# Kernel optimization log

Measured on AMD Instinct MI355X. Metric: run time of the kernel, lower is better.

## Reference

```python
import jax, jax.numpy as jnp
import numpy as np

B, S, D = 4, 2048, 1024
H = 16
HD = D // H
FF = 4096
EPS = 1e-5

def _layernorm(x, g, b):
    mu = jnp.mean(x, axis=-1, keepdims=True)
    var = jnp.mean(jnp.square(x - mu), axis=-1, keepdims=True)
    return (x - mu) * jax.lax.rsqrt(var + EPS) * g + b

def setup_inputs() -> dict:
    key = jax.random.key(0)
    ks = jax.random.split(key, 12)
    s_attn = 1.0 / np.sqrt(D)
    s_ff1 = 1.0 / np.sqrt(D)
    s_ff2 = 1.0 / np.sqrt(FF)
    return {
        "x": jax.random.normal(ks[0], (B, S, D), jnp.float32),
        "ln1_g": jnp.ones((D,), jnp.float32),
        "ln1_b": jnp.zeros((D,), jnp.float32),
        "ln2_g": jnp.ones((D,), jnp.float32),
        "ln2_b": jnp.zeros((D,), jnp.float32),
        "Wq": jax.random.normal(ks[1], (D, D), jnp.float32) * s_attn,
        "Wk": jax.random.normal(ks[2], (D, D), jnp.float32) * s_attn,
        "Wv": jax.random.normal(ks[3], (D, D), jnp.float32) * s_attn,
        "Wo": jax.random.normal(ks[4], (D, D), jnp.float32) * s_attn,
        "W1": jax.random.normal(ks[5], (D, FF), jnp.float32) * s_ff1,
        "b1": jnp.zeros((FF,), jnp.float32),
        "W2": jax.random.normal(ks[6], (FF, D), jnp.float32) * s_ff2,
        "b2": jnp.zeros((D,), jnp.float32),
    }

def reference(x, ln1_g, ln1_b, ln2_g, ln2_b, Wq, Wk, Wv, Wo, W1, b1, W2, b2):
    # pre-LN self-attention (y = x), mask=None, dropout=0, attn proj bias=False
    h = _layernorm(x, ln1_g, ln1_b)                      # [B,S,D]
    q = (h @ Wq).reshape(B, S, H, HD).transpose(0, 2, 1, 3)  # [B,H,S,HD]
    k = (h @ Wk).reshape(B, S, H, HD).transpose(0, 2, 1, 3)
    v = (h @ Wv).reshape(B, S, H, HD).transpose(0, 2, 1, 3)
    scores = jnp.einsum('bhqd,bhkd->bhqk', q, k) / np.sqrt(HD)  # [B,H,S,S]
    attn = jax.nn.softmax(scores, axis=-1)
    o = jnp.einsum('bhqk,bhkd->bhqd', attn, v)           # [B,H,S,HD]
    o = o.transpose(0, 2, 1, 3).reshape(B, S, D) @ Wo
    x = x + o
    h2 = _layernorm(x, ln2_g, ln2_b)
    ff = jax.nn.relu(h2 @ W1 + b1) @ W2 + b2             # note: second FC also has relu per FC default
    ff = jax.nn.relu(ff)
    return x + ff
```

## Files before the change

kernel.cpp:

```cpp
#include <hip/hip_runtime.h>
#include <hip/hip_bf16.h>
#include <cstdint>
#include <cstddef>

typedef unsigned short u16;
typedef unsigned int u32;
typedef __bf16 bf16x2 __attribute__((ext_vector_type(2)));
typedef __bf16 bf16x8 __attribute__((ext_vector_type(8)));
typedef float f32x4 __attribute__((ext_vector_type(4)));

#define NB 4
#define NS 2048
#define ND 1024
#define NH 16
#define NHD 64
#define NFF 4096
#define CSC 0.18033688011112042f

#if __has_builtin(__builtin_amdgcn_exp2f)
#define EXP2(x) __builtin_amdgcn_exp2f(x)
#else
#define EXP2(x) exp2f(x)
#endif

__device__ __forceinline__ u16 f2b(float f) {
  union { bf16x2 h; u32 u; } v;
  v.h[0] = (__bf16)f; v.h[1] = (__bf16)f;
  return (u16)(v.u & 0xFFFF);
}
__device__ __forceinline__ u32 pack2(float a, float b) {
  union { bf16x2 h; u32 u; } v;
  v.h[0] = (__bf16)a; v.h[1] = (__bf16)b;
  return v.u;
}

__device__ __forceinline__ void async_copy16(const u16* g, u16* l) {
  __builtin_amdgcn_global_load_lds(
      (const __attribute__((address_space(1))) void*)(const void*)g,
      (__attribute__((address_space(3))) void*)(void*)l, 16, 0, 0);
}

__global__ __launch_bounds__(256) void transpose_f2b(const float* __restrict__ in,
                                                     u16* __restrict__ out,
                                                     int R, int C) {
  __shared__ float tile[32][33];
  const int bx = blockIdx.x * 32;
  const int by = blockIdx.y * 32;
  const int tx = threadIdx.x & 31, ty = threadIdx.x >> 5;
#pragma unroll
  for (int i = 0; i < 32; i += 8)
    tile[ty + i][tx] = in[(size_t)(by + ty + i) * C + bx + tx];
  __syncthreads();
#pragma unroll
  for (int i = 0; i < 32; i += 8)
    out[(size_t)(bx + ty + i) * R + by + tx] = f2b(tile[tx][ty + i]);
}

__global__ __launch_bounds__(256) void ln_kernel(const float* __restrict__ xin,
                                                 const float* __restrict__ g,
                                                 const float* __restrict__ b,
                                                 u16* __restrict__ out) {
  const int row = blockIdx.x;
  const int tid = threadIdx.x;
  const float* p = xin + (size_t)row * ND;
  float v[4];
#pragma unroll
  for (int i = 0; i < 4; i++) v[i] = p[tid + 256 * i];
  float s = 0.f, ss = 0.f;
#pragma unroll
  for (int i = 0; i < 4; i++) { s += v[i]; ss += v[i] * v[i]; }
  for (int off = 32; off > 0; off >>= 1) {
    s += __shfl_down(s, off);
    ss += __shfl_down(ss, off);
  }
  __shared__ float r0[4], r1[4];
  const int w = tid >> 6;
  if ((tid & 63) == 0) { r0[w] = s; r1[w] = ss; }
  __syncthreads();
  s = r0[0] + r0[1] + r0[2] + r0[3];
  ss = r1[0] + r1[1] + r1[2] + r1[3];
  const float mu = s * (1.f / ND);
  const float var = ss * (1.f / ND) - mu * mu;
  const float rstd = rsqrtf(var + 1e-5f);
  u16* o = out + (size_t)row * ND;
#pragma unroll
  for (int i = 0; i < 4; i++) {
    const int c = tid + 256 * i;
    o[c] = f2b((v[i] - mu) * rstd * g[c] + b[c]);
  }
}

template <int OUT_MODE, int RES_MODE, bool BIAS, bool RELU>
__global__ __launch_bounds__(256) void gemm_bt(const u16* __restrict__ A,
                                               const u16* __restrict__ Bt,
                                               const float* __restrict__ bias,
                                               const float* __restrict__ res,
                                               void* __restrict__ out,
                                               u16* __restrict__ outK,
                                               u16* __restrict__ outV,
                                               int M, int N, int K) {
  __shared__ __align__(16) u16 lA[2][128 * 64];
  __shared__ __align__(16) u16 lB[2][128 * 64];
  const int tid = threadIdx.x;
  const int bm = blockIdx.y * 128, bn = blockIdx.x * 128;
  const int w = tid >> 6, lane = tid & 63, quad = lane >> 4, l16 = lane & 15;
  const int wm = (w & 1) * 64, wn = (w >> 1) * 64;
  const int sw = l16 & 7;

  f32x4 acc[4][4];
#pragma unroll
  for (int i = 0; i < 4; i++)
#pragma unroll
    for (int j = 0; j < 4; j++) acc[i][j] = (f32x4){0.f, 0.f, 0.f, 0.f};

  const int srow = w * 8 + (lane >> 3);
  const int sch = (lane & 7) ^ ((lane >> 3) & 7);
  const u16* Ap = A + (size_t)(bm + srow) * K + sch * 8;
  const u16* Bp = Bt + (size_t)(bn + srow) * K + sch * 8;
  const int NT = K >> 6;

#pragma unroll
  for (int c = 0; c < 4; c++)
    async_copy16(Ap + (size_t)c * 32 * K, &lA[0][(c * 32 + w * 8) * 64]);
#pragma unroll
  for (int c = 0; c < 4; c++)
    async_copy16(Bp + (size_t)c * 32 * K, &lB[0][(c * 32 + w * 8) * 64]);

  for (int kt = 0; kt < NT; ++kt) {
    const int cur = kt & 1;
    __syncthreads();
    if (kt + 1 < NT) {
      const size_t koff = (size_t)(kt + 1) * 64;
#pragma unroll
      for (int c = 0; c < 4; c++)
        async_copy16(Ap + (size_t)c * 32 * K + koff,
                     &lA[cur ^ 1][(c * 32 + w * 8) * 64]);
#pragma unroll
      for (int c = 0; c < 4; c++)
        async_copy16(Bp + (size_t)c * 32 * K + koff,
                     &lB[cur ^ 1][(c * 32 + w * 8) * 64]);
    }
    const u16* lAc = lA[cur];
    const u16* lBc = lB[cur];
#pragma unroll
    for (int x = 0; x < 2; x++) {
      bf16x8 af[4], bf[4];
#pragma unroll
      for (int i = 0; i < 4; i++)
        af[i] = *(const bf16x8*)&lAc[(wm + i * 16 + l16) * 64 + ((x * 4 + quad) ^ sw) * 8];
#pragma unroll
      for (int j = 0; j < 4; j++)
        bf[j] = *(const bf16x8*)&lBc[(wn + j * 16 + l16) * 64 + ((x * 4 + quad) ^ sw) * 8];
#pragma unroll
      for (int i = 0; i < 4; i++)
#pragma unroll
        for (int j = 0; j < 4; j++)
          acc[i][j] = __builtin_amdgcn_mfma_f32_16x16x32_bf16(af[i], bf[j], acc[i][j], 0, 0, 0);
    }
  }

  if constexpr (OUT_MODE == 3) {
    const int m0 = bm + wm;
#pragma unroll
    for (int i = 0; i < 4; i++) {
#pragma unroll
      for (int j = 0; j < 4; j++) {
        const int n = bn + wn + j * 16 + l16;
        const int mB = m0 + i * 16 + quad * 4;
        const int bb = mB >> 11, s = mB & 2047;
        if (bn < 1024) {
          const int hh = n >> 6, hd = n & 63;
          u16* o = (u16*)out + (((size_t)(bb * NH + hh) * NS + s) * NHD + hd);
#pragma unroll
          for (int r = 0; r < 4; r++) o[(size_t)r * NHD] = f2b(acc[i][j][r] * CSC);
        } else if (bn < 2048) {
          const int nk = n - 1024;
          const int hh = nk >> 6, hd = nk & 63;
          u16* o = outK + (((size_t)(bb * NH + hh) * NS + s) * NHD + hd);
#pragma unroll
          for (int r = 0; r < 4; r++) o[(size_t)r * NHD] = f2b(acc[i][j][r]);
        } else {
          const int nv = n - 2048;
          const int hh = nv >> 6, hd = nv & 63;
          uint2 pk = make_uint2(pack2(acc[i][j][0], acc[i][j][1]),
                                pack2(acc[i][j][2], acc[i][j][3]));
          *(uint2*)&outV[((size_t)(bb * NH + hh) * NHD + hd) * NS + s] = pk;
        }
      }
    }
  } else {
#pragma unroll
    for (int i = 0; i < 4; i++) {
#pragma unroll
      for (int r = 0; r < 4; r++) {
        const int m = bm + wm + i * 16 + quad * 4 + r;
#pragma unroll
        for (int j = 0; j < 4; j++) {
          const int n = bn + wn + j * 16 + l16;
          float vv = acc[i][j][r];
          if constexpr (BIAS) vv += bias[n];
          if constexpr (RELU) vv = fmaxf(vv, 0.f);
          if constexpr (RES_MODE == 1) vv += res[(size_t)m * N + n];
          if constexpr (OUT_MODE == 0) {
            ((u16*)out)[(size_t)m * N + n] = f2b(vv);
          } else {
            ((float*)out)[(size_t)m * N + n] = vv;
          }
        }
      }
    }
  }
}

#define OSTR 72
__global__ __launch_bounds__(256, 4) void attn_kernel(const u16* __restrict__ Q,
                                                      const u16* __restrict__ K,
                                                      const u16* __restrict__ VT,
                                                      u16* __restrict__ O) {
  __shared__ __align__(16) u16 lK[128 * 64];
  __shared__ __align__(16) u16 lV[64 * 128];
  const int tid = threadIdx.x;
  const int w = tid >> 6, lane = tid & 63, quad = lane >> 4, l16 = lane & 15;
  const int sw = l16 & 7;

  const int bid = blockIdx.x;
  const int xcd = bid & 7, slot = bid >> 3;
  const int bh = xcd + 8 * (slot >> 5);
  const int q0 = (slot & 31) * 64;
  const size_t base = (size_t)bh * NS * NHD;

  const u16* qrow = Q + base + (size_t)(q0 + w * 16 + l16) * NHD;
  bf16x8 qf[2];
  qf[0] = *(const bf16x8*)(qrow + quad * 8);
  qf[1] = *(const bf16x8*)(qrow + 32 + quad * 8);

  const int krow = w * 8 + (lane >> 3);
  const int kch = (lane & 7) ^ ((lane >> 3) & 7);
  const int vrow = w * 4 + (lane >> 4);
  const int vch = (lane & 15) ^ (vrow & 7);
  const u16* kp = K + base + (size_t)krow * 64 + kch * 8;
  const u16* vp = VT + base + (size_t)vrow * NS + vch * 8;

  float l_i = 0.f;
  f32x4 oa[4];
#pragma unroll
  for (int jo = 0; jo < 4; jo++) oa[jo] = (f32x4){0.f, 0.f, 0.f, 0.f};

  for (int kt = 0; kt < NS / 128; ++kt) {
    __syncthreads();
#pragma unroll
    for (int c = 0; c < 4; c++)
      async_copy16(kp + (size_t)c * 32 * 64, &lK[(c * 32 + w * 8) * 64]);
#pragma unroll
    for (int c = 0; c < 4; c++)
      async_copy16(vp + (size_t)c * 16 * NS, &lV[(c * 16 + w * 4) * 128]);
    __syncthreads();
    kp += 128 * 64;
    vp += 128;

    f32x4 sc[8];
#pragma unroll
    for (int j = 0; j < 8; j++) sc[j] = (f32x4){0.f, 0.f, 0.f, 0.f};
#pragma unroll
    for (int x = 0; x < 2; x++)
#pragma unroll
      for (int j = 0; j < 8; j++) {
        bf16x8 kf = *(const bf16x8*)&lK[(j * 16 + l16) * 64 + ((x * 4 + quad) ^ sw) * 8];
        sc[j] = __builtin_amdgcn_mfma_f32_16x16x32_bf16(kf, qf[x], sc[j], 0, 0, 0);
      }

    float rsum = 0.f;
#pragma unroll
    for (int j = 0; j < 8; j++) {
#pragma unroll
      for (int r = 0; r < 4; r++) sc[j][r] = EXP2(sc[j][r]);
      rsum += (sc[j][0] + sc[j][1]) + (sc[j][2] + sc[j][3]);
    }
    rsum += __shfl_xor(rsum, 16);
    rsum += __shfl_xor(rsum, 32);
    l_i += rsum;

#pragma unroll
    for (int x = 0; x < 4; x++) {
      u32 A0 = pack2(sc[2 * x][0], sc[2 * x][1]);
      u32 A1 = pack2(sc[2 * x][2], sc[2 * x][3]);
      u32 B0 = pack2(sc[2 * x + 1][0], sc[2 * x + 1][1]);
      u32 B1 = pack2(sc[2 * x + 1][2], sc[2 * x + 1][3]);
      asm("v_permlane32_swap_b32 %0, %1" : "+v"(A0), "+v"(B0));
      asm("v_permlane32_swap_b32 %0, %1" : "+v"(A1), "+v"(B1));
      asm("v_permlane16_swap_b32 %0, %1" : "+v"(A0), "+v"(B0));
      asm("v_permlane16_swap_b32 %0, %1" : "+v"(A1), "+v"(B1));
      union { u32 u[4]; bf16x8 h; } bq;
      bq.u[0] = A0; bq.u[1] = A1; bq.u[2] = B0; bq.u[3] = B1;
#pragma unroll
      for (int jo = 0; jo < 4; jo++) {
        bf16x8 av = *(const bf16x8*)&lV[(jo * 16 + l16) * 128 + ((x * 4 + quad) ^ sw) * 8];
        oa[jo] = __builtin_amdgcn_mfma_f32_16x16x32_bf16(av, bq.h, oa[jo], 0, 0, 0);
      }
    }
  }

  __syncthreads();
  const float inv = 1.f / l_i;
  u16* lo = &lK[w * 16 * OSTR];
#pragma unroll
  for (int jo = 0; jo < 4; jo++)
#pragma unroll
    for (int pr = 0; pr < 2; pr++)
      *(u32*)&lo[l16 * OSTR + jo * 16 + quad * 4 + pr * 2] =
          pack2(oa[jo][2 * pr] * inv, oa[jo][2 * pr + 1] * inv);

  const int bb = bh >> 4, hh = bh & 15;
#pragma unroll
  for (int t = 0; t < 2; t++) {
    const int row = t * 8 + (lane >> 3);
    const int seg = lane & 7;
    bf16x8 ov = *(const bf16x8*)&lo[row * OSTR + seg * 8];
    const int srow = q0 + w * 16 + row;
    *(int4*)&O[((size_t)bb * NS + srow) * ND + hh * 64 + seg * 8] = *(int4*)&ov;
  }
}

extern "C" void kernel_launch(void* const* d_in, const int* in_sizes, int n_in,
                              void* d_out, int out_size, void* d_ws, size_t ws_size,
                              hipStream_t stream) {
  (void)in_sizes; (void)n_in; (void)out_size; (void)ws_size;
  const float* x = (const float*)d_in[0];
  const float* ln1g = (const float*)d_in[1];
  const float* ln1b = (const float*)d_in[2];
  const float* ln2g = (const float*)d_in[3];
  const float* ln2b = (const float*)d_in[4];
  const float* Wq = (const float*)d_in[5];
  const float* Wk = (const float*)d_in[6];
  const float* Wv = (const float*)d_in[7];
  const float* Wo = (const float*)d_in[8];
  const float* W1 = (const float*)d_in[9];
  const float* b1 = (const float*)d_in[10];
  const float* W2 = (const float*)d_in[11];
  const float* b2 = (const float*)d_in[12];

  u16* ws = (u16*)d_ws;
  u16* h     = ws;
  u16* WqkvT = ws + (size_t)8  * 1048576;
  u16* WoT   = ws + (size_t)11 * 1048576;
  u16* W1T   = ws + (size_t)12 * 1048576;
  u16* W2T   = ws + (size_t)16 * 1048576;
  u16* qb    = ws + (size_t)20 * 1048576;
  u16* kb    = ws + (size_t)28 * 1048576;
  u16* vt    = ws + (size_t)36 * 1048576;
  u16* ob    = ws + (size_t)44 * 1048576;
  float* x2  = (float*)(ws + (size_t)52 * 1048576);
  u16* ff    = qb;
  u16* h2    = h;

  const int M = NB * NS;

  transpose_f2b<<<dim3(32, 32), 256, 0, stream>>>(Wq, WqkvT, ND, ND);
  transpose_f2b<<<dim3(32, 32), 256, 0, stream>>>(Wk, WqkvT + (size_t)1024 * 1024, ND, ND);
  transpose_f2b<<<dim3(32, 32), 256, 0, stream>>>(Wv, WqkvT + (size_t)2048 * 1024, ND, ND);
  transpose_f2b<<<dim3(32, 32), 256, 0, stream>>>(Wo, WoT, ND, ND);
  transpose_f2b<<<dim3(128, 32), 256, 0, stream>>>(W1, W1T, ND, NFF);
  transpose_f2b<<<dim3(32, 128), 256, 0, stream>>>(W2, W2T, NFF, ND);

  ln_kernel<<<M, 256, 0, stream>>>(x, ln1g, ln1b, h);

  gemm_bt<3, 0, false, false><<<dim3(24, 64), 256, 0, stream>>>(
      h, WqkvT, nullptr, nullptr, qb, kb, vt, M, 3072, ND);

  attn_kernel<<<dim3(2048), 256, 0, stream>>>(qb, kb, vt, ob);

  gemm_bt<2, 1, false, false><<<dim3(8, 64), 256, 0, stream>>>(
      ob, WoT, nullptr, x, x2, nullptr, nullptr, M, ND, ND);

  ln_kernel<<<M, 256, 0, stream>>>(x2, ln2g, ln2b, h2);

  gemm_bt<0, 0, true, true><<<dim3(32, 64), 256, 0, stream>>>(
      h2, W1T, b1, nullptr, ff, nullptr, nullptr, M, NFF, ND);

  gemm_bt<2, 1, true, true><<<dim3(8, 64), 256, 0, stream>>>(
      ff, W2T, b2, x2, d_out, nullptr, nullptr, M, ND, NFF);
}
```

Baseline: 509.4 us.

## Add 256x256-tile pipelined GEMM kernel for the FF1 projection

Adds a new 512-thread GEMM that computes a 256x256 output tile per workgroup, uses double-buffered LDS filled by async global-to-LDS copies, and interleaves the prefetch of later K tiles with the MFMA phases. It also remaps workgroups across the XCDs. This replaces the previous generic gemm_bt launch for the h2 @ W1 + b1, ReLU stage. The aim is more data reuse per tile and better overlap of loads with compute. In exchange it needs large LDS and many accumulator registers per thread, which limits occupancy, and the hand-written waitcnt and barrier schedule is fragile.

```diff
diff --git a/kernel.cpp b/kernel.cpp
--- a/kernel.cpp
+++ b/kernel.cpp
@@ -38,6 +38,11 @@
   __builtin_amdgcn_global_load_lds(
       (const __attribute__((address_space(1))) void*)(const void*)g,
       (__attribute__((address_space(3))) void*)(void*)l, 16, 0, 0);
+}
+
+template <int N> __device__ __forceinline__ void vmw() {
+  if constexpr (N == 0) asm volatile("s_waitcnt vmcnt(0)" ::: "memory");
+  else if constexpr (N == 6) asm volatile("s_waitcnt vmcnt(6)" ::: "memory");
 }
 
 __global__ __launch_bounds__(256) void transpose_f2b(const float* __restrict__ in,
@@ -207,6 +212,125 @@
             ((float*)out)[(size_t)m * N + n] = vv;
           }
         }
+      }
+    }
+  }
+}
+
+template <bool BIAS, bool RELU>
+__global__ __launch_bounds__(512, 2) void gemm_8ph(const u16* __restrict__ A,
+                                                   const u16* __restrict__ Bt,
+                                                   const float* __restrict__ bias,
+                                                   u16* __restrict__ out,
+                                                   int M, int N, int K) {
+  __shared__ __align__(16) u16 lA[2][256 * 64];
+  __shared__ __align__(16) u16 lB[2][256 * 64];
+  const int tid = threadIdx.x;
+  const int w = tid >> 6, lane = tid & 63, quad = lane >> 4, l16 = lane & 15;
+  const int sw = l16 & 7;
+  const int wr = w >> 2, wc = w & 3;
+
+  const int nb = gridDim.x, chunk = nb >> 3;
+  const int wg = ((int)blockIdx.x & 7) * chunk + ((int)blockIdx.x >> 3);
+  const int nby = M >> 8;
+  const int bx = wg / nby, by = wg % nby;
+  const int bm = by * 256, bn = bx * 256;
+
+  f32x4 acc[8][4];
+#pragma unroll
+  for (int i = 0; i < 8; i++)
+#pragma unroll
+    for (int j = 0; j < 4; j++) acc[i][j] = (f32x4){0.f, 0.f, 0.f, 0.f};
+
+  const int srow = w * 8 + (lane >> 3);
+  const int sch = (lane & 7) ^ ((lane >> 3) & 7);
+  const u16* Ap = A + (size_t)(bm + srow) * K + sch * 8;
+  const u16* Bp = Bt + (size_t)(bn + srow) * K + sch * 8;
+  const int NT = K >> 6;
+
+  auto stA = [&](int t, int h) {
+    async_copy16(Ap + (size_t)(h * 64) * K + (size_t)t * 64,
+                 &lA[t & 1][(h * 64 + w * 8) * 64]);
+  };
+  auto stB = [&](int t, int h) {
+    async_copy16(Bp + (size_t)(h * 64) * K + (size_t)t * 64,
+                 &lB[t & 1][(h * 64 + w * 8) * 64]);
+  };
+
+  stA(0, 0); stA(0, 1); stA(0, 2); stA(0, 3);
+  stB(0, 0); stB(0, 1); stB(0, 2); stB(0, 3);
+  stB(1, 0); stB(1, 1); stB(1, 2); stB(1, 3);
+  stA(1, 0); stA(1, 2);
+  vmw<6>();
+  __builtin_amdgcn_s_barrier();
+  __builtin_amdgcn_sched_barrier(0);
+
+  for (int kt = 0; kt < NT; ++kt) {
+    const u16* lAc = lA[kt & 1];
+    const u16* lBc = lB[kt & 1];
+    bf16x8 bfr[4][2];
+#pragma unroll
+    for (int p = 0; p < 4; ++p) {
+      bf16x8 af[2][2];
+#pragma unroll
+      for (int ii = 0; ii < 2; ii++)
+#pragma unroll
+        for (int x = 0; x < 2; x++)
+          af[ii][x] = *(const bf16x8*)&lAc[(wr * 128 + (p * 2 + ii) * 16 + l16) * 64 +
+                                           ((x * 4 + quad) ^ sw) * 8];
+      if (p == 0) {
+#pragma unroll
+        for (int j = 0; j < 4; j++)
+#pragma unroll
+          for (int x = 0; x < 2; x++)
+            bfr[j][x] = *(const bf16x8*)&lBc[(wc * 64 + j * 16 + l16) * 64 +
+                                             ((x * 4 + quad) ^ sw) * 8];
+        if (kt + 1 < NT) { stA(kt + 1, 1); stA(kt + 1, 3); }
+      } else if (p == 1) {
+        if (kt + 2 < NT) { stB(kt + 2, 0); stB(kt + 2, 1); }
+      } else if (p == 2) {
+        if (kt + 2 < NT) { stB(kt + 2, 2); stB(kt + 2, 3); }
+      } else {
+        if (kt + 2 < NT) { stA(kt + 2, 0); stA(kt + 2, 2); }
+      }
+      __builtin_amdgcn_s_barrier();
+      __builtin_amdgcn_sched_barrier(0);
+      __builtin_amdgcn_s_setprio(1);
+#pragma unroll
+      for (int ii = 0; ii < 2; ii++)
+#pragma unroll
+        for (int j = 0; j < 4; j++)
+#pragma unroll
+          for (int x = 0; x < 2; x++)
+            acc[p * 2 + ii][j] = __builtin_amdgcn_mfma_f32_16x16x32_bf16(
+                af[ii][x], bfr[j][x], acc[p * 2 + ii][j], 0, 0, 0);
+      __builtin_amdgcn_s_setprio(0);
+      if (p == 3) {
+        if (kt + 2 < NT) {
+          vmw<6>();
+          __builtin_amdgcn_sched_barrier(0);
+        } else if (kt + 1 < NT) {
+          vmw<0>();
+          __builtin_amdgcn_sched_barrier(0);
+        }
+      }
+      __builtin_amdgcn_s_barrier();
+      __builtin_amdgcn_sched_barrier(0);
+    }
+  }
+
+#pragma unroll
+  for (int i = 0; i < 8; i++) {
+#pragma unroll
+    for (int r = 0; r < 4; r++) {
+      const int m = bm + wr * 128 + i * 16 + quad * 4 + r;
+#pragma unroll
+      for (int j = 0; j < 4; j++) {
+        const int n = bn + wc * 64 + j * 16 + l16;
+        float vv = acc[i][j][r];
+        if constexpr (BIAS) vv += bias[n];
+        if constexpr (RELU) vv = fmaxf(vv, 0.f);
+        out[(size_t)m * N + n] = f2b(vv);
       }
     }
   }
@@ -374,8 +498,7 @@
 
   ln_kernel<<<M, 256, 0, stream>>>(x2, ln2g, ln2b, h2);
 
-  gemm_bt<0, 0, true, true><<<dim3(32, 64), 256, 0, stream>>>(
-      h2, W1T, b1, nullptr, ff, nullptr, nullptr, M, NFF, ND);
+  gemm_8ph<true, true><<<512, 512, 0, stream>>>(h2, W1T, b1, ff, M, NFF, ND);
 
   gemm_bt<2, 1, true, true><<<dim3(8, 64), 256, 0, stream>>>(
       ff, W2T, b2, x2, d_out, nullptr, nullptr, M, ND, NFF);
```

After: 507.7 us. No clear change (-0.3%).
